# Performance work log

Hardware: AMD Instinct MI355X
Metric: run time of the kernel (lower is better)

Reference implementation:

```python
import jax, jax.numpy as jnp
import numpy as np

N_NODES = 50000
N_EDGES = 1600000
IN_CH = 64
EDGE_DIM = 32
NUM_HID = 256
NUM_CLASSES = 16
NUM_GRAPHS = 512


def setup_inputs() -> dict:
    key = jax.random.key(0)
    ks = jax.random.split(key, 16)
    z_dim = 2 * IN_CH + EDGE_DIM
    s = lambda k, shp, fan: jax.random.normal(k, shp, dtype=jnp.float32) * (1.0 / np.sqrt(fan))
    return {
        "x": jax.random.normal(ks[0], (N_NODES, IN_CH), dtype=jnp.float32),
        "edge_index": jax.random.randint(ks[1], (2, N_EDGES), 0, N_NODES, dtype=jnp.int64),
        "edge_attr": jax.random.normal(ks[2], (N_EDGES, EDGE_DIM), dtype=jnp.float32),
        "batch": jnp.sort(jax.random.randint(ks[3], (N_NODES,), 0, NUM_GRAPHS, dtype=jnp.int64)),
        # CGConv layer 1 (lin_f: gate, lin_s: filter)
        "w_f1": s(ks[4], (IN_CH, z_dim), z_dim), "b_f1": jnp.zeros((IN_CH,), jnp.float32),
        "w_s1": s(ks[5], (IN_CH, z_dim), z_dim), "b_s1": jnp.zeros((IN_CH,), jnp.float32),
        # CGConv layer 2
        "w_f2": s(ks[6], (IN_CH, z_dim), z_dim), "b_f2": jnp.zeros((IN_CH,), jnp.float32),
        "w_s2": s(ks[7], (IN_CH, z_dim), z_dim), "b_s2": jnp.zeros((IN_CH,), jnp.float32),
        # MLP
        "w1": s(ks[8], (NUM_HID, IN_CH), IN_CH), "b1": jnp.zeros((NUM_HID,), jnp.float32),
        "w2": s(ks[9], (NUM_CLASSES, NUM_HID), NUM_HID), "b2": jnp.zeros((NUM_CLASSES,), jnp.float32),
    }


def _cgconv(x, src, dst, edge_attr, w_f, b_f, w_s, b_s, inv_deg):
    # z = [x_i, x_j, e_ij] per edge (j -> i), shape [E, 2C+D]
    z = jnp.concatenate([x[dst], x[src], edge_attr], axis=1)
    msg = jax.nn.sigmoid(z @ w_f.T + b_f) * jax.nn.softplus(z @ w_s.T + b_s)
    agg = jax.ops.segment_sum(msg, dst, num_segments=N_NODES) * inv_deg[:, None]
    return agg + x  # residual connection in CGConv


def reference(x, edge_index, edge_attr, batch,
              w_f1, b_f1, w_s1, b_s1, w_f2, b_f2, w_s2, b_s2,
              w1, b1, w2, b2):
    src, dst = edge_index[0], edge_index[1]
    deg = jax.ops.segment_sum(jnp.ones((src.shape[0],), x.dtype), dst, num_segments=N_NODES)
    inv_deg = 1.0 / jnp.maximum(deg, 1.0)

    h = _cgconv(x, src, dst, edge_attr, w_f1, b_f1, w_s1, b_s1, inv_deg)
    h = _cgconv(h, src, dst, edge_attr, w_f2, b_f2, w_s2, b_s2, inv_deg)

    # scatter_mean over graphs
    gsum = jax.ops.segment_sum(h, batch, num_segments=NUM_GRAPHS)
    gcnt = jax.ops.segment_sum(jnp.ones((h.shape[0],), h.dtype), batch, num_segments=NUM_GRAPHS)
    g = gsum / jnp.maximum(gcnt, 1.0)[:, None]

    out = jax.nn.relu(g @ w1.T + b1) @ w2.T + b2
    return jax.nn.log_softmax(out, axis=1)
```

## Files before the change

### kernel.cpp

```cpp
#include <hip/hip_runtime.h>
#include <hip/hip_bf16.h>

#define N_NODES 50000
#define N_EDGES 1600000
#define IN_CH 64
#define NUM_HID 256
#define NUM_CLASSES 16
#define NUM_GRAPHS 512
#define NBS 196

typedef short bf16x8 __attribute__((ext_vector_type(8)));
typedef float f32x4 __attribute__((ext_vector_type(4)));

#if __has_builtin(__builtin_amdgcn_rcpf)
#define RCPF(x) __builtin_amdgcn_rcpf(x)
#else
#define RCPF(x) (1.0f / (x))
#endif

__device__ inline unsigned short f2b(float f) {
    unsigned int u = __float_as_uint(f);
    unsigned int r = (u + 0x7FFF + ((u >> 16) & 1)) >> 16;
    return (unsigned short)r;
}
__device__ inline float b2f(unsigned short u) {
    return __uint_as_float(((unsigned int)u) << 16);
}

__global__ void prep_w_kernel(const float* __restrict__ wf1, const float* __restrict__ ws1,
                              const float* __restrict__ wf2, const float* __restrict__ ws2,
                              unsigned short* __restrict__ wb1, unsigned short* __restrict__ wb2) {
    int i = blockIdx.x * 256 + threadIdx.x;
    if (i >= 128 * 160) return;
    int r = i / 160, k = i - r * 160;
    wb1[i] = f2b(r < 64 ? wf1[r * 160 + k] : ws1[(r - 64) * 160 + k]);
    wb2[i] = f2b(r < 64 ? wf2[r * 160 + k] : ws2[(r - 64) * 160 + k]);
}

__global__ void prep_x_kernel(const float4* __restrict__ x, unsigned short* __restrict__ xb) {
    int i = blockIdx.x * 256 + threadIdx.x;
    if (i >= N_NODES * 16) return;
    float4 v = x[i];
    ushort4 u; u.x = f2b(v.x); u.y = f2b(v.y); u.z = f2b(v.z); u.w = f2b(v.w);
    *(ushort4*)(xb + i * 4) = u;
}

__global__ void hist_kernel(const int* __restrict__ ei, int* __restrict__ cnt) {
    int i = blockIdx.x * 256 + threadIdx.x;
    if (i < N_EDGES) atomicAdd(&cnt[ei[N_EDGES + i]], 1);
}

__global__ void bsum_kernel(const int* __restrict__ cnt, int* __restrict__ bsum) {
    __shared__ int sm[256];
    int i = blockIdx.x * 256 + threadIdx.x;
    sm[threadIdx.x] = (i < N_NODES) ? cnt[i] : 0;
    __syncthreads();
    for (int off = 128; off > 0; off >>= 1) {
        if (threadIdx.x < off) sm[threadIdx.x] += sm[threadIdx.x + off];
        __syncthreads();
    }
    if (threadIdx.x == 0) bsum[blockIdx.x] = sm[0];
}

__global__ void bscan_kernel(const int* __restrict__ bsum, int* __restrict__ boffs) {
    __shared__ int sm[256];
    int t = threadIdx.x;
    int v = (t < NBS) ? bsum[t] : 0;
    sm[t] = v; __syncthreads();
    for (int off = 1; off < 256; off <<= 1) {
        int u = (t >= off) ? sm[t - off] : 0;
        __syncthreads();
        sm[t] += u;
        __syncthreads();
    }
    if (t < NBS) boffs[t] = sm[t] - v;
}

__global__ void apply_kernel(const int* __restrict__ cnt, const int* __restrict__ boffs,
                             int* __restrict__ cursor, float* __restrict__ invdeg) {
    __shared__ int sm[256];
    int t = threadIdx.x, i = blockIdx.x * 256 + t;
    int c = (i < N_NODES) ? cnt[i] : 0;
    sm[t] = c; __syncthreads();
    for (int off = 1; off < 256; off <<= 1) {
        int u = (t >= off) ? sm[t - off] : 0;
        __syncthreads();
        sm[t] += u;
        __syncthreads();
    }
    if (i < N_NODES) {
        cursor[i] = boffs[blockIdx.x] + sm[t] - c;
        invdeg[i] = 1.0f / fmaxf((float)c, 1.0f);
    }
}

__global__ void scatter_kernel(const int* __restrict__ ei, int* __restrict__ cursor,
                               const float* __restrict__ ea,
                               int2* __restrict__ sed, unsigned short* __restrict__ eab) {
    int e = blockIdx.x * 256 + threadIdx.x;
    if (e >= N_EDGES) return;
    int s = ei[e], d = ei[N_EDGES + e];
    int p = atomicAdd(&cursor[d], 1);
    sed[p] = make_int2(s, d);
    const float4* src = (const float4*)(ea + (size_t)e * 32);
    unsigned short* dst = eab + (size_t)p * 32;
    #pragma unroll
    for (int j = 0; j < 8; ++j) {
        float4 v = src[j];
        ushort4 u; u.x = f2b(v.x); u.y = f2b(v.y); u.z = f2b(v.z); u.w = f2b(v.w);
        *(ushort4*)(dst + j * 4) = u;
    }
}

__global__ __launch_bounds__(256, 2)
void edge_mfma(const unsigned short* __restrict__ xb,
               const int2* __restrict__ sed, const unsigned short* __restrict__ eab,
               const unsigned short* __restrict__ wb,
               const float* __restrict__ bfv, const float* __restrict__ bsv,
               float* __restrict__ agg)
{
    __shared__ __align__(16) unsigned short Zd[2][64 * 64];
    __shared__ __align__(16) unsigned short Zs[2][64 * 64];
    __shared__ __align__(16) unsigned short Ze[2][64 * 32];
    __shared__ int dstl[2][64];

    const int tid = threadIdx.x;
    const int w = tid >> 6, lane = tid & 63, lr = lane & 15, lq = lane >> 4;
    const int eh = (w >> 1) * 32, chh = (w & 1) * 32;

    bf16x8 B[2][2][5];
    #pragma unroll
    for (int mat = 0; mat < 2; ++mat)
        #pragma unroll
        for (int n = 0; n < 2; ++n)
            #pragma unroll
            for (int ks = 0; ks < 5; ++ks)
                B[mat][n][ks] = *(const bf16x8*)(wb + (size_t)(mat * 64 + chh + n * 16 + lr) * 160 + ks * 32 + lq * 8);

    float biasF[2], biasS[2];
    #pragma unroll
    for (int n = 0; n < 2; ++n) { biasF[n] = bfv[chh + n * 16 + lr]; biasS[n] = bsv[chh + n * 16 + lr]; }

    const int rA0 = tid >> 3, cA0 = tid & 7;
    const int rA1 = rA0 + 32;
    const int rE = tid >> 2, cE = tid & 3;
    const int dcA0 = cA0 ^ (rA0 & 7), dcA1 = cA0 ^ (rA1 & 7);
    const int dcE8 = (cE ^ ((rE >> 1) & 3)) * 8;

    const int NT = N_EDGES / 64;
    const int nblk = gridDim.x;

    bf16x8 vd0, vd1, vs0, vs1, veb;
    int dl = 0;

    #define ISSUE_A(T) do { \
        int e0_ = (T) * 64; \
        int2 sA0 = sed[e0_ + rA0]; \
        vd0 = *(const bf16x8*)(xb + (size_t)sA0.y * 64 + dcA0 * 8); \
        vs0 = *(const bf16x8*)(xb + (size_t)sA0.x * 64 + dcA0 * 8); \
        if (tid < 64) dl = sed[e0_ + tid].y; \
    } while (0)
    #define ISSUE_B(T) do { \
        int e0_ = (T) * 64; \
        int2 sA1 = sed[e0_ + rA1]; \
        vd1 = *(const bf16x8*)(xb + (size_t)sA1.y * 64 + dcA1 * 8); \
        vs1 = *(const bf16x8*)(xb + (size_t)sA1.x * 64 + dcA1 * 8); \
        veb = *(const bf16x8*)(eab + (size_t)(e0_ + rE) * 32 + dcE8); \
    } while (0)

    #define WRITE(PAR) do { \
        *(bf16x8*)&Zd[PAR][rA0 * 64 + cA0 * 8] = vd0; \
        *(bf16x8*)&Zd[PAR][rA1 * 64 + cA0 * 8] = vd1; \
        *(bf16x8*)&Zs[PAR][rA0 * 64 + cA0 * 8] = vs0; \
        *(bf16x8*)&Zs[PAR][rA1 * 64 + cA0 * 8] = vs1; \
        *(bf16x8*)&Ze[PAR][rE * 32 + cE * 8] = veb; \
        if (tid < 64) dstl[PAR][tid] = dl; \
    } while (0)

    #define SOFT_BARRIER() do { \
        asm volatile("s_waitcnt lgkmcnt(0)" ::: "memory"); \
        __builtin_amdgcn_s_barrier(); \
    } while (0)

    int t = blockIdx.x;
    if (t < NT) { ISSUE_A(t); ISSUE_B(t); WRITE(0); }
    SOFT_BARRIER();
    int par = 0;

    for (; t < NT; t += nblk) {
        int tn = t + nblk;
        bool pf = tn < NT;
        if (pf) ISSUE_A(tn);

        f32x4 aF[2][2] = {}; f32x4 aS[2][2] = {};
        const int r0 = eh + lr, r1 = eh + 16 + lr;
        #pragma unroll
        for (int ks = 0; ks < 5; ++ks) {
            bf16x8 a0, a1;
            if (ks < 2) {
                int j = ks * 4 + lq;
                a0 = *(const bf16x8*)&Zd[par][r0 * 64 + ((j ^ (r0 & 7)) * 8)];
                a1 = *(const bf16x8*)&Zd[par][r1 * 64 + ((j ^ (r1 & 7)) * 8)];
            } else if (ks < 4) {
                int j = (ks - 2) * 4 + lq;
                a0 = *(const bf16x8*)&Zs[par][r0 * 64 + ((j ^ (r0 & 7)) * 8)];
                a1 = *(const bf16x8*)&Zs[par][r1 * 64 + ((j ^ (r1 & 7)) * 8)];
            } else {
                a0 = *(const bf16x8*)&Ze[par][r0 * 32 + ((lq ^ ((r0 >> 1) & 3)) * 8)];
                a1 = *(const bf16x8*)&Ze[par][r1 * 32 + ((lq ^ ((r1 >> 1) & 3)) * 8)];
            }
            aF[0][0] = __builtin_amdgcn_mfma_f32_16x16x32_bf16(a0, B[0][0][ks], aF[0][0], 0, 0, 0);
            aF[0][1] = __builtin_amdgcn_mfma_f32_16x16x32_bf16(a0, B[0][1][ks], aF[0][1], 0, 0, 0);
            aF[1][0] = __builtin_amdgcn_mfma_f32_16x16x32_bf16(a1, B[0][0][ks], aF[1][0], 0, 0, 0);
            aF[1][1] = __builtin_amdgcn_mfma_f32_16x16x32_bf16(a1, B[0][1][ks], aF[1][1], 0, 0, 0);
            aS[0][0] = __builtin_amdgcn_mfma_f32_16x16x32_bf16(a0, B[1][0][ks], aS[0][0], 0, 0, 0);
            aS[0][1] = __builtin_amdgcn_mfma_f32_16x16x32_bf16(a0, B[1][1][ks], aS[0][1], 0, 0, 0);
            aS[1][0] = __builtin_amdgcn_mfma_f32_16x16x32_bf16(a1, B[1][0][ks], aS[1][0], 0, 0, 0);
            aS[1][1] = __builtin_amdgcn_mfma_f32_16x16x32_bf16(a1, B[1][1][ks], aS[1][1], 0, 0, 0);
        }

        if (pf) ISSUE_B(tn);

        float v0[8], v1[8];
        #pragma unroll
        for (int m = 0; m < 2; ++m)
            #pragma unroll
            for (int i = 0; i < 4; ++i) {
                {
                    float f = aF[m][0][i] + biasF[0];
                    float s = aS[m][0][i] + biasS[0];
                    float sig = RCPF(1.0f + __expf(-f));
                    float sp = fmaxf(s, 0.0f) + __logf(1.0f + __expf(-fabsf(s)));
                    v0[m * 4 + i] = sig * sp;
                }
                {
                    float f = aF[m][1][i] + biasF[1];
                    float s = aS[m][1][i] + biasS[1];
                    float sig = RCPF(1.0f + __expf(-f));
                    float sp = fmaxf(s, 0.0f) + __logf(1.0f + __expf(-fabsf(s)));
                    v1[m * 4 + i] = sig * sp;
                }
            }

        {
            int rel = lane & 31;
            int dme = dstl[par][eh + rel];
            int dprev = (rel == 0) ? ~dme : dstl[par][eh + rel - 1];
            unsigned long long bmask = __ballot(dme != dprev) & 0xFFFFFFFFull;
            while (bmask) {
                int lo = (int)__builtin_ctzll(bmask);
                bmask &= bmask - 1;
                int hi = bmask ? (int)__builtin_ctzll(bmask) : 32;
                int dst = dstl[par][eh + lo];
                float t0 = 0.0f, t1 = 0.0f;
                #pragma unroll
                for (int m = 0; m < 2; ++m)
                    #pragma unroll
                    for (int i = 0; i < 4; ++i) {
                        int r = m * 16 + lq * 4 + i;
                        bool in = (r >= lo) && (r < hi);
                        t0 += in ? v0[m * 4 + i] : 0.0f;
                        t1 += in ? v1[m * 4 + i] : 0.0f;
                    }
                t0 += __shfl_xor(t0, 16); t0 += __shfl_xor(t0, 32);
                t1 += __shfl_xor(t1, 16); t1 += __shfl_xor(t1, 32);
                if (lq < 2) {
                    int c = chh + (lq << 4) + lr;
                    float val = lq ? t1 : t0;
                    atomicAdd(&agg[(size_t)dst * 64 + c], val);
                }
            }
        }

        if (pf) WRITE(par ^ 1);
        SOFT_BARRIER();
        par ^= 1;
    }
    #undef ISSUE_A
    #undef ISSUE_B
    #undef WRITE
    #undef SOFT_BARRIER
}

__global__ void resid2_kernel(const float4* __restrict__ agg, const float* __restrict__ inv_deg,
                              const float4* __restrict__ x, unsigned short* __restrict__ hb)
{
    int i = blockIdx.x * 256 + threadIdx.x;
    if (i >= N_NODES * 16) return;
    int n = i >> 4;
    float iv = inv_deg[n];
    float4 a = agg[i], xv = x[i];
    ushort4 u;
    u.x = f2b(a.x * iv + xv.x); u.y = f2b(a.y * iv + xv.y);
    u.z = f2b(a.z * iv + xv.z); u.w = f2b(a.w * iv + xv.w);
    *(ushort4*)(hb + i * 4) = u;
}

__global__ void pool2_kernel(const float* __restrict__ agg, const float* __restrict__ inv_deg,
                             const unsigned short* __restrict__ hb, const int* __restrict__ batch,
                             float* __restrict__ gsum, float* __restrict__ gcnt)
{
    const int ch = threadIdx.x & 63, sub = threadIdx.x >> 6;
    const int base = blockIdx.x * 64 + sub * 16;
    float acc = 0.0f;
    int gcur = -1, rl = 0;
    #pragma unroll
    for (int j = 0; j < 16; ++j) {
        int n = base + j;
        if (n >= N_NODES) break;
        int g = batch[n];
        float v = agg[(size_t)n * 64 + ch] * inv_deg[n] + b2f(hb[(size_t)n * 64 + ch]);
        if (g != gcur) {
            if (gcur >= 0) {
                atomicAdd(&gsum[gcur * 64 + ch], acc);
                if (ch == 0) atomicAdd(&gcnt[gcur], (float)rl);
            }
            gcur = g; acc = v; rl = 1;
        } else {
            acc += v; rl++;
        }
    }
    if (gcur >= 0) {
        atomicAdd(&gsum[gcur * 64 + ch], acc);
        if (ch == 0) atomicAdd(&gcnt[gcur], (float)rl);
    }
}

__global__ __launch_bounds__(64)
void head_kernel(const float* __restrict__ gsum, const float* __restrict__ gcnt,
                 const float* __restrict__ w1, const float* __restrict__ b1,
                 const float* __restrict__ w2, const float* __restrict__ b2,
                 float* __restrict__ out)
{
    __shared__ float gv[64];
    __shared__ float hid[256];
    __shared__ float outv[16];
    const int g = blockIdx.x, t = threadIdx.x;
    float cnt = fmaxf(gcnt[g], 1.0f);
    gv[t] = gsum[g * 64 + t] / cnt;
    __syncthreads();
    #pragma unroll
    for (int r = 0; r < 4; ++r) {
        int c = t + r * 64;
        float acc = b1[c];
        const float4* wr = (const float4*)(w1 + c * 64);
        const float4* gvv = (const float4*)gv;
        #pragma unroll
        for (int k = 0; k < 16; ++k) {
            float4 wv = wr[k], xv = gvv[k];
            acc += wv.x * xv.x + wv.y * xv.y + wv.z * xv.z + wv.w * xv.w;
        }
        hid[c] = fmaxf(acc, 0.0f);
    }
    __syncthreads();
    if (t < 16) {
        float acc = b2[t];
        const float4* wr = (const float4*)(w2 + t * 256);
        const float4* hv = (const float4*)hid;
        for (int k = 0; k < 64; ++k) {
            float4 wv = wr[k], xv = hv[k];
            acc += wv.x * xv.x + wv.y * xv.y + wv.z * xv.z + wv.w * xv.w;
        }
        outv[t] = acc;
    }
    __syncthreads();
    if (t < 16) {
        float m = outv[0];
        #pragma unroll
        for (int j = 1; j < 16; ++j) m = fmaxf(m, outv[j]);
        float ssum = 0.0f;
        #pragma unroll
        for (int j = 0; j < 16; ++j) ssum += expf(outv[j] - m);
        out[g * 16 + t] = outv[t] - m - logf(ssum);
    }
}

extern "C" void kernel_launch(void* const* d_in, const int* in_sizes, int n_in,
                              void* d_out, int out_size, void* d_ws, size_t ws_size,
                              hipStream_t stream)
{
    const float* x     = (const float*)d_in[0];
    const int*   ei    = (const int*)d_in[1];
    const float* ea    = (const float*)d_in[2];
    const int*   batch = (const int*)d_in[3];
    const float* wf1 = (const float*)d_in[4];
    const float* bf1 = (const float*)d_in[5];
    const float* ws1 = (const float*)d_in[6];
    const float* bs1 = (const float*)d_in[7];
    const float* wf2 = (const float*)d_in[8];
    const float* bf2 = (const float*)d_in[9];
    const float* ws2 = (const float*)d_in[10];
    const float* bs2 = (const float*)d_in[11];
    const float* w1 = (const float*)d_in[12];
    const float* b1 = (const float*)d_in[13];
    const float* w2 = (const float*)d_in[14];
    const float* b2 = (const float*)d_in[15];
    float* out = (float*)d_out;

    char* ws = (char*)d_ws;
    int*   cnt    = (int*)(ws + 0x0000000);
    int*   cursor = (int*)(ws + 0x0040000);
    float* invdeg = (float*)(ws + 0x0080000);
    int*   bsum   = (int*)(ws + 0x00C0000);
    int*   boffs  = (int*)(ws + 0x00C1000);
    int2*  sed    = (int2*)(ws + 0x0100000);
    unsigned short* xb  = (unsigned short*)(ws + 0x1500000);
    unsigned short* hb  = (unsigned short*)(ws + 0x1C00000);
    float* agg = (float*)(ws + 0x2300000);
    unsigned short* wb1 = (unsigned short*)(ws + 0x3000000);
    unsigned short* wb2 = (unsigned short*)(ws + 0x3010000);
    float* gsum = (float*)(ws + 0x3020000);
    float* gcnt = (float*)(ws + 0x3040000);
    unsigned short* eab = (unsigned short*)(ws + 0x3100000);

    hipMemsetAsync(cnt, 0, 200000, stream);
    hipMemsetAsync(agg, 0, 12800000, stream);
    hipMemsetAsync(gsum, 0, 131072 + 2048, stream);

    prep_w_kernel<<<80, 256, 0, stream>>>(wf1, ws1, wf2, ws2, wb1, wb2);
    prep_x_kernel<<<3125, 256, 0, stream>>>((const float4*)x, xb);
    hist_kernel<<<6250, 256, 0, stream>>>(ei, cnt);
    bsum_kernel<<<NBS, 256, 0, stream>>>(cnt, bsum);
    bscan_kernel<<<1, 256, 0, stream>>>(bsum, boffs);
    apply_kernel<<<NBS, 256, 0, stream>>>(cnt, boffs, cursor, invdeg);
    scatter_kernel<<<6250, 256, 0, stream>>>(ei, cursor, ea, sed, eab);

    edge_mfma<<<1024, 256, 0, stream>>>(xb, sed, eab, wb1, bf1, bs1, agg);
    resid2_kernel<<<3125, 256, 0, stream>>>((const float4*)agg, invdeg, (const float4*)x, hb);
    hipMemsetAsync(agg, 0, 12800000, stream);
    edge_mfma<<<1024, 256, 0, stream>>>(hb, sed, eab, wb2, bf2, bs2, agg);
    pool2_kernel<<<782, 256, 0, stream>>>(agg, invdeg, hb, batch, gsum, gcnt);
    head_kernel<<<NUM_GRAPHS, 64, 0, stream>>>(gsum, gcnt, w1, b1, w2, b2, out);
}
```

Baseline: 610.4 us.

## Repartition edge MFMA so each wave owns 16 channels across all 64 edges

Each of the four waves now computes 16 output channels for all 64 edges of a tile, instead of a 32-edge by 32-channel quadrant. Destination indices are read straight from global memory into registers and compared with shuffles, which removes the dstl shared buffer. Segments are now detected over 64 edges, so fewer atomics are issued per run, and the shared-memory write of the first prefetch half is moved earlier. In exchange, each wave does more LDS reads of A fragments (4 row blocks per wave), and the run loop can execute more iterations per wave.

New measurement: 622.3 us. Within noise of the previous version (+2.0%).

```diff
diff --git a/kernel.cpp b/kernel.cpp
--- a/kernel.cpp
+++ b/kernel.cpp
@@ -122,24 +122,20 @@
     __shared__ __align__(16) unsigned short Zd[2][64 * 64];
     __shared__ __align__(16) unsigned short Zs[2][64 * 64];
     __shared__ __align__(16) unsigned short Ze[2][64 * 32];
-    __shared__ int dstl[2][64];
 
     const int tid = threadIdx.x;
     const int w = tid >> 6, lane = tid & 63, lr = lane & 15, lq = lane >> 4;
-    const int eh = (w >> 1) * 32, chh = (w & 1) * 32;
-
-    bf16x8 B[2][2][5];
+    const int chw = w * 16;
+
+    bf16x8 B[2][5];
     #pragma unroll
     for (int mat = 0; mat < 2; ++mat)
         #pragma unroll
-        for (int n = 0; n < 2; ++n)
-            #pragma unroll
-            for (int ks = 0; ks < 5; ++ks)
-                B[mat][n][ks] = *(const bf16x8*)(wb + (size_t)(mat * 64 + chh + n * 16 + lr) * 160 + ks * 32 + lq * 8);
-
-    float biasF[2], biasS[2];
-    #pragma unroll
-    for (int n = 0; n < 2; ++n) { biasF[n] = bfv[chh + n * 16 + lr]; biasS[n] = bsv[chh + n * 16 + lr]; }
+        for (int ks = 0; ks < 5; ++ks)
+            B[mat][ks] = *(const bf16x8*)(wb + (size_t)(mat * 64 + chw + lr) * 160 + ks * 32 + lq * 8);
+
+    const float biasF = bfv[chw + lr];
+    const float biasS = bsv[chw + lr];
 
     const int rA0 = tid >> 3, cA0 = tid & 7;
     const int rA1 = rA0 + 32;
@@ -150,15 +146,14 @@
     const int NT = N_EDGES / 64;
     const int nblk = gridDim.x;
 
-    bf16x8 vd0, vd1, vs0, vs1, veb;
-    int dl = 0;
+    bf16x8 vd0, vs0;
+    bf16x8 vd1, vs1, veb;
 
     #define ISSUE_A(T) do { \
         int e0_ = (T) * 64; \
         int2 sA0 = sed[e0_ + rA0]; \
         vd0 = *(const bf16x8*)(xb + (size_t)sA0.y * 64 + dcA0 * 8); \
         vs0 = *(const bf16x8*)(xb + (size_t)sA0.x * 64 + dcA0 * 8); \
-        if (tid < 64) dl = sed[e0_ + tid].y; \
     } while (0)
     #define ISSUE_B(T) do { \
         int e0_ = (T) * 64; \
@@ -167,118 +162,100 @@
         vs1 = *(const bf16x8*)(xb + (size_t)sA1.x * 64 + dcA1 * 8); \
         veb = *(const bf16x8*)(eab + (size_t)(e0_ + rE) * 32 + dcE8); \
     } while (0)
-
-    #define WRITE(PAR) do { \
+    #define WRITE_A(PAR) do { \
         *(bf16x8*)&Zd[PAR][rA0 * 64 + cA0 * 8] = vd0; \
+        *(bf16x8*)&Zs[PAR][rA0 * 64 + cA0 * 8] = vs0; \
+    } while (0)
+    #define WRITE_B(PAR) do { \
         *(bf16x8*)&Zd[PAR][rA1 * 64 + cA0 * 8] = vd1; \
-        *(bf16x8*)&Zs[PAR][rA0 * 64 + cA0 * 8] = vs0; \
         *(bf16x8*)&Zs[PAR][rA1 * 64 + cA0 * 8] = vs1; \
         *(bf16x8*)&Ze[PAR][rE * 32 + cE * 8] = veb; \
-        if (tid < 64) dstl[PAR][tid] = dl; \
     } while (0)
-
     #define SOFT_BARRIER() do { \
         asm volatile("s_waitcnt lgkmcnt(0)" ::: "memory"); \
         __builtin_amdgcn_s_barrier(); \
     } while (0)
 
     int t = blockIdx.x;
-    if (t < NT) { ISSUE_A(t); ISSUE_B(t); WRITE(0); }
+    if (t < NT) { ISSUE_A(t); WRITE_A(0); ISSUE_B(t); WRITE_B(0); }
     SOFT_BARRIER();
     int par = 0;
 
     for (; t < NT; t += nblk) {
         int tn = t + nblk;
         bool pf = tn < NT;
+        int dme = sed[t * 64 + lane].y;
         if (pf) ISSUE_A(tn);
 
-        f32x4 aF[2][2] = {}; f32x4 aS[2][2] = {};
-        const int r0 = eh + lr, r1 = eh + 16 + lr;
+        f32x4 aF[4] = {}; f32x4 aS[4] = {};
         #pragma unroll
         for (int ks = 0; ks < 5; ++ks) {
-            bf16x8 a0, a1;
-            if (ks < 2) {
-                int j = ks * 4 + lq;
-                a0 = *(const bf16x8*)&Zd[par][r0 * 64 + ((j ^ (r0 & 7)) * 8)];
-                a1 = *(const bf16x8*)&Zd[par][r1 * 64 + ((j ^ (r1 & 7)) * 8)];
-            } else if (ks < 4) {
-                int j = (ks - 2) * 4 + lq;
-                a0 = *(const bf16x8*)&Zs[par][r0 * 64 + ((j ^ (r0 & 7)) * 8)];
-                a1 = *(const bf16x8*)&Zs[par][r1 * 64 + ((j ^ (r1 & 7)) * 8)];
-            } else {
-                a0 = *(const bf16x8*)&Ze[par][r0 * 32 + ((lq ^ ((r0 >> 1) & 3)) * 8)];
-                a1 = *(const bf16x8*)&Ze[par][r1 * 32 + ((lq ^ ((r1 >> 1) & 3)) * 8)];
+            bf16x8 a[4];
+            #pragma unroll
+            for (int m = 0; m < 4; ++m) {
+                const int rm = m * 16 + lr;
+                if (ks < 2) {
+                    int j = ks * 4 + lq;
+                    a[m] = *(const bf16x8*)&Zd[par][rm * 64 + ((j ^ (rm & 7)) * 8)];
+                } else if (ks < 4) {
+                    int j = (ks - 2) * 4 + lq;
+                    a[m] = *(const bf16x8*)&Zs[par][rm * 64 + ((j ^ (rm & 7)) * 8)];
+                } else {
+                    a[m] = *(const bf16x8*)&Ze[par][rm * 32 + ((lq ^ ((rm >> 1) & 3)) * 8)];
+                }
             }
-            aF[0][0] = __builtin_amdgcn_mfma_f32_16x16x32_bf16(a0, B[0][0][ks], aF[0][0], 0, 0, 0);
-            aF[0][1] = __builtin_amdgcn_mfma_f32_16x16x32_bf16(a0, B[0][1][ks], aF[0][1], 0, 0, 0);
-            aF[1][0] = __builtin_amdgcn_mfma_f32_16x16x32_bf16(a1, B[0][0][ks], aF[1][0], 0, 0, 0);
-            aF[1][1] = __builtin_amdgcn_mfma_f32_16x16x32_bf16(a1, B[0][1][ks], aF[1][1], 0, 0, 0);
-            aS[0][0] = __builtin_amdgcn_mfma_f32_16x16x32_bf16(a0, B[1][0][ks], aS[0][0], 0, 0, 0);
-            aS[0][1] = __builtin_amdgcn_mfma_f32_16x16x32_bf16(a0, B[1][1][ks], aS[0][1], 0, 0, 0);
-            aS[1][0] = __builtin_amdgcn_mfma_f32_16x16x32_bf16(a1, B[1][0][ks], aS[1][0], 0, 0, 0);
-            aS[1][1] = __builtin_amdgcn_mfma_f32_16x16x32_bf16(a1, B[1][1][ks], aS[1][1], 0, 0, 0);
+            #pragma unroll
+            for (int m = 0; m < 4; ++m) {
+                aF[m] = __builtin_amdgcn_mfma_f32_16x16x32_bf16(a[m], B[0][ks], aF[m], 0, 0, 0);
+                aS[m] = __builtin_amdgcn_mfma_f32_16x16x32_bf16(a[m], B[1][ks], aS[m], 0, 0, 0);
+            }
         }
 
-        if (pf) ISSUE_B(tn);
-
-        float v0[8], v1[8];
-        #pragma unroll
-        for (int m = 0; m < 2; ++m)
+        if (pf) { WRITE_A(par ^ 1); ISSUE_B(tn); }
+
+        float val[16];
+        #pragma unroll
+        for (int m = 0; m < 4; ++m)
             #pragma unroll
             for (int i = 0; i < 4; ++i) {
-                {
-                    float f = aF[m][0][i] + biasF[0];
-                    float s = aS[m][0][i] + biasS[0];
-                    float sig = RCPF(1.0f + __expf(-f));
-                    float sp = fmaxf(s, 0.0f) + __logf(1.0f + __expf(-fabsf(s)));
-                    v0[m * 4 + i] = sig * sp;
-                }
-                {
-                    float f = aF[m][1][i] + biasF[1];
-                    float s = aS[m][1][i] + biasS[1];
-                    float sig = RCPF(1.0f + __expf(-f));
-                    float sp = fmaxf(s, 0.0f) + __logf(1.0f + __expf(-fabsf(s)));
-                    v1[m * 4 + i] = sig * sp;
-                }
+                float f = aF[m][i] + biasF;
+                float s = aS[m][i] + biasS;
+                float sig = RCPF(1.0f + __expf(-f));
+                float sp = fmaxf(s, 0.0f) + __logf(1.0f + __expf(-fabsf(s)));
+                val[m * 4 + i] = sig * sp;
             }
 
         {
-            int rel = lane & 31;
-            int dme = dstl[par][eh + rel];
-            int dprev = (rel == 0) ? ~dme : dstl[par][eh + rel - 1];
-            unsigned long long bmask = __ballot(dme != dprev) & 0xFFFFFFFFull;
+            int dprev = __shfl(dme, lane - 1);
+            unsigned long long bmask = __ballot((lane == 0) || (dme != dprev));
             while (bmask) {
                 int lo = (int)__builtin_ctzll(bmask);
                 bmask &= bmask - 1;
-                int hi = bmask ? (int)__builtin_ctzll(bmask) : 32;
-                int dst = dstl[par][eh + lo];
-                float t0 = 0.0f, t1 = 0.0f;
+                int hi = bmask ? (int)__builtin_ctzll(bmask) : 64;
+                int dst = __shfl(dme, lo);
+                float t0 = 0.0f;
                 #pragma unroll
-                for (int m = 0; m < 2; ++m)
+                for (int m = 0; m < 4; ++m)
                     #pragma unroll
                     for (int i = 0; i < 4; ++i) {
                         int r = m * 16 + lq * 4 + i;
-                        bool in = (r >= lo) && (r < hi);
-                        t0 += in ? v0[m * 4 + i] : 0.0f;
-                        t1 += in ? v1[m * 4 + i] : 0.0f;
+                        t0 += ((r >= lo) && (r < hi)) ? val[m * 4 + i] : 0.0f;
                     }
-                t0 += __shfl_xor(t0, 16); t0 += __shfl_xor(t0, 32);
-                t1 += __shfl_xor(t1, 16); t1 += __shfl_xor(t1, 32);
-                if (lq < 2) {
-                    int c = chh + (lq << 4) + lr;
-                    float val = lq ? t1 : t0;
-                    atomicAdd(&agg[(size_t)dst * 64 + c], val);
-                }
+                t0 += __shfl_xor(t0, 16);
+                t0 += __shfl_xor(t0, 32);
+                if (lq == 0)
+                    atomicAdd(&agg[(size_t)dst * 64 + chw + lr], t0);
             }
         }
 
-        if (pf) WRITE(par ^ 1);
+        if (pf) WRITE_B(par ^ 1);
         SOFT_BARRIER();
         par ^= 1;
     }
     #undef ISSUE_A
     #undef ISSUE_B
-    #undef WRITE
+    #undef WRITE_A
+    #undef WRITE_B
     #undef SOFT_BARRIER
 }
 
```
